# Kernel tuning notes

Hardware: AMD Instinct MI355X
Metric: run time of the kernel (lower is better)

## Reference

```python
import jax, jax.numpy as jnp
import numpy as np

N_NODES = 100000
N_EDGES = 1600000
IN_C, HID_C, OUT_C = 128, 256, 128


def setup_inputs() -> dict:
    key = jax.random.key(0)
    ks = jax.random.split(key, 8)
    x = jax.random.normal(ks[0], (N_NODES, IN_C), dtype=jnp.float32)
    edge_row = jax.random.randint(ks[1], (N_EDGES,), 0, N_NODES, dtype=jnp.int32)
    edge_col = jax.random.randint(ks[2], (N_EDGES,), 0, N_NODES, dtype=jnp.int32)
    # normalized adjacency values (e.g. D^-1/2 A D^-1/2 entries), positive
    edge_vals = jax.random.uniform(ks[3], (N_EDGES,), dtype=jnp.float32) * 0.1
    # torch Linear weights: y = x @ W.T + b (xavier scale)
    W1 = jax.random.normal(ks[4], (HID_C, IN_C), dtype=jnp.float32) * (2.0 / (IN_C + HID_C)) ** 0.5
    b1 = jnp.zeros((HID_C,), dtype=jnp.float32)
    W2 = jax.random.normal(ks[5], (HID_C, HID_C), dtype=jnp.float32) * (1.0 / HID_C) ** 0.5
    b2 = jnp.zeros((HID_C,), dtype=jnp.float32)
    W3 = jax.random.normal(ks[6], (OUT_C, HID_C), dtype=jnp.float32) * (2.0 / (HID_C + OUT_C)) ** 0.5
    b3 = jnp.zeros((OUT_C,), dtype=jnp.float32)
    return {"x": x, "edge_row": edge_row, "edge_col": edge_col, "edge_vals": edge_vals,
            "W1": W1, "b1": b1, "W2": W2, "b2": b2, "W3": W3, "b3": b3}


def reference(x, edge_row, edge_col, edge_vals, W1, b1, W2, b2, W3, b3):
    n = x.shape[0]

    def spmm(h):
        # out[i] = sum over edges e with row[e]==i of vals[e] * h[col[e]]
        msgs = h[edge_col] * edge_vals[:, None]          # [E, C]
        return jax.ops.segment_sum(msgs, edge_row, num_segments=n)

    h = jax.nn.relu(spmm(x) @ W1.T + b1)                 # GCNConv 1 + relu
    h = jax.nn.relu(spmm(h) @ W2.T + b2)                 # GCNConv 2 + relu
    h = spmm(h) @ W3.T + b3                              # GCNConv 3 (no act)
    # F.normalize: L2 along dim=1 with eps clamp 1e-12
    norm = jnp.linalg.norm(h, axis=1, keepdims=True)
    return h / jnp.maximum(norm, 1e-12)
```

## Files before the change

kernel.cpp:

```cpp
#include <hip/hip_runtime.h>
#include <hip/hip_bf16.h>

#define N_NODES 100000
#define N_EDGES 1600000
#define IN_C 128
#define HID_C 256
#define OUT_C 128

typedef __attribute__((ext_vector_type(8))) short bf16x8;
typedef __attribute__((ext_vector_type(4))) float f32x4;
typedef __attribute__((ext_vector_type(2))) float f32x2;

static __device__ __forceinline__ short f2bf(float f) {
    union { float f; unsigned u; } x{f};
    unsigned r = (x.u + 0x7fffu + ((x.u >> 16) & 1u)) >> 16;
    return (short)r;
}
static __device__ __forceinline__ f32x2 bfpair(unsigned d) {
    union { unsigned u; float f; } lo, hi;
    lo.u = d << 16;
    hi.u = d & 0xffff0000u;
    return f32x2{lo.f, hi.f};
}

__global__ void hist_rank(const int* __restrict__ rows, int* __restrict__ deg,
                          int* __restrict__ rank, int E)
{
    int e = blockIdx.x * blockDim.x + threadIdx.x;
    if (e < E) rank[e] = atomicAdd(&deg[rows[e]], 1);
}

#define SCAN_BLOCK 256
#define SCAN_ELEMS 1024

__global__ __launch_bounds__(SCAN_BLOCK) void scan1(const int* __restrict__ deg,
                                                    int* __restrict__ excl,
                                                    int* __restrict__ bsum, int N)
{
    __shared__ int sh[SCAN_BLOCK];
    int t = threadIdx.x;
    int base = blockIdx.x * SCAN_ELEMS + t * 4;
    int v[4];
    #pragma unroll
    for (int i = 0; i < 4; ++i) {
        int idx = base + i;
        v[i] = (idx < N) ? deg[idx] : 0;
    }
    int s = v[0] + v[1] + v[2] + v[3];
    sh[t] = s;
    __syncthreads();
    for (int d = 1; d < SCAN_BLOCK; d <<= 1) {
        int add = (t >= d) ? sh[t - d] : 0;
        __syncthreads();
        sh[t] += add;
        __syncthreads();
    }
    int p = sh[t] - s;
    #pragma unroll
    for (int i = 0; i < 4; ++i) {
        int idx = base + i;
        if (idx < N) excl[idx] = p;
        p += v[i];
    }
    if (t == SCAN_BLOCK - 1) bsum[blockIdx.x] = sh[t];
}

__global__ void scan2(const int* __restrict__ bsum, int* __restrict__ boff, int NB)
{
    __shared__ int sh[128];
    int t = threadIdx.x;
    int v = (t < NB) ? bsum[t] : 0;
    sh[t] = v;
    __syncthreads();
    for (int d = 1; d < 128; d <<= 1) {
        int add = (t >= d) ? sh[t - d] : 0;
        __syncthreads();
        sh[t] += add;
        __syncthreads();
    }
    if (t < NB) boff[t] = sh[t] - v;
}

__global__ void scan3(int* __restrict__ row_start, const int* __restrict__ boff, int N, int E)
{
    int i = blockIdx.x * blockDim.x + threadIdx.x;
    if (i < N) {
        row_start[i] = row_start[i] + boff[i >> 10];
    } else if (i == N) {
        row_start[N] = E;
    }
}

__global__ void scatter_edges(const int* __restrict__ rows, const int* __restrict__ cols,
                              const float* __restrict__ vals, const int* __restrict__ row_start,
                              const int* __restrict__ rank, int2* __restrict__ epk, int E)
{
    int e = blockIdx.x * blockDim.x + threadIdx.x;
    if (e < E) {
        int pos = row_start[rows[e]] + rank[e];
        epk[pos] = int2{cols[e], __float_as_int(vals[e])};
    }
}

__global__ void cast_all(const float* __restrict__ s0, short* __restrict__ d0, int n0,
                         const float* __restrict__ s1, short* __restrict__ d1, int n1,
                         const float* __restrict__ s2, short* __restrict__ d2, int n2,
                         const float* __restrict__ s3, short* __restrict__ d3, int n3)
{
    int i = (blockIdx.x * blockDim.x + threadIdx.x) * 4;
    const float* s; short* d;
    if (i < n0) { s = s0; d = d0; }
    else if ((i -= n0) < n1) { s = s1; d = d1; }
    else if ((i -= n1) < n2) { s = s2; d = d2; }
    else if ((i -= n2) < n3) { s = s3; d = d3; }
    else return;
    float4 v = *(const float4*)(s + i);
    *(short4*)(d + i) = short4{f2bf(v.x), f2bf(v.y), f2bf(v.z), f2bf(v.w)};
}

template<int B, int ND>
static __device__ __forceinline__ void spmm_batch(
    const unsigned* __restrict__ Hb, const int2* __restrict__ epk,
    int j, int loff, f32x2* acc)
{
    int2 e[B];
    #pragma unroll
    for (int b = 0; b < B; ++b) e[b] = epk[j + b];
    uint2 g[B];
    #pragma unroll
    for (int b = 0; b < B; ++b) {
        const unsigned* p = Hb + (size_t)e[b].x * (64 * ND) + loff;
        if constexpr (ND == 2) g[b] = *(const uint2*)p;
        else                   g[b].x = *p;
    }
    #pragma unroll
    for (int b = 0; b < B; ++b) {
        float v = __int_as_float(e[b].y);
        acc[0] += v * bfpair(g[b].x);
        if constexpr (ND == 2) acc[1] += v * bfpair(g[b].y);
    }
}

template<int C, int MODE>
__global__ __launch_bounds__(256) void spmm_gather(
    const short* __restrict__ H, const int* __restrict__ row_start,
    const int2* __restrict__ epk, void* __restrict__ outv,
    const float* __restrict__ bias, int N)
{
    constexpr int PL = C / 64;
    constexpr int ND = PL / 2;
    int wid = threadIdx.x >> 6;
    int lane = threadIdx.x & 63;
    int row = blockIdx.x * 4 + wid;
    if (row >= N) return;
    int j = row_start[row];
    int end = row_start[row + 1];
    const unsigned* Hb = (const unsigned*)H;
    const int loff = lane * ND;

    f32x2 acc[ND];
    #pragma unroll
    for (int d = 0; d < ND; ++d) acc[d] = f32x2{0.f, 0.f};

    for (; j + 8 <= end; j += 8) spmm_batch<8, ND>(Hb, epk, j, loff, acc);
    if (j + 4 <= end) { spmm_batch<4, ND>(Hb, epk, j, loff, acc); j += 4; }
    if (j + 2 <= end) { spmm_batch<2, ND>(Hb, epk, j, loff, acc); j += 2; }
    if (j < end)      { spmm_batch<1, ND>(Hb, epk, j, loff, acc); }

    if constexpr (MODE == 0) {
        unsigned od[ND];
        #pragma unroll
        for (int d = 0; d < ND; ++d)
            od[d] = (unsigned)(unsigned short)f2bf(acc[d].x)
                  | ((unsigned)(unsigned short)f2bf(acc[d].y) << 16);
        unsigned* orow = (unsigned*)outv + (size_t)row * (64 * ND) + loff;
        if constexpr (ND == 2) *(uint2*)orow = uint2{od[0], od[1]};
        else                   *orow = od[0];
    } else {
        int ch = lane * 2;
        float o0 = acc[0].x + bias[ch];
        float o1 = acc[0].y + bias[ch + 1];
        float ss = o0 * o0 + o1 * o1;
        #pragma unroll
        for (int d = 1; d < 64; d <<= 1)
            ss += __shfl_xor(ss, d);
        float s = 1.0f / fmaxf(sqrtf(ss), 1e-12f);
        *(float2*)((float*)outv + (size_t)row * C + ch) = float2{o0 * s, o1 * s};
    }
}

template<int K, int M, bool RELU, bool BIAS>
__global__ __launch_bounds__(256) void gemm_bf16(
    const short* __restrict__ A, const short* __restrict__ W,
    const float* __restrict__ bias, short* __restrict__ Y, int N)
{
    constexpr int BK = 32;
    constexpr int PAD = 8;
    __shared__ short As[128][BK + PAD];
    __shared__ short Ws[64][BK + PAD];

    const int tid = threadIdx.x;
    const int wid = tid >> 6;
    const int lane = tid & 63;
    const int wm = wid & 1;
    const int wn = wid >> 1;
    const int l15 = lane & 15;
    const int quad = lane >> 4;
    const int bn = blockIdx.x * 128;
    const int bm = blockIdx.y * 64;

    f32x4 acc[4][2] = {};

    for (int k0 = 0; k0 < K; k0 += BK) {
        #pragma unroll
        for (int c = 0; c < 2; ++c) {
            int chunk = tid + c * 256;
            int row = chunk >> 2;
            int koff = (chunk & 3) * 8;
            int gr = bn + row;
            ulonglong2 v = {0ull, 0ull};
            if (gr < N) v = *(const ulonglong2*)(A + (size_t)gr * K + k0 + koff);
            *(ulonglong2*)&As[row][koff] = v;
        }
        {
            int row = tid >> 2;
            int koff = (tid & 3) * 8;
            ulonglong2 v = *(const ulonglong2*)(W + (size_t)(bm + row) * K + k0 + koff);
            *(ulonglong2*)&Ws[row][koff] = v;
        }
        __syncthreads();

        bf16x8 aF[4], bF[2];
        #pragma unroll
        for (int mt = 0; mt < 4; ++mt)
            aF[mt] = *(const bf16x8*)&As[wm * 64 + mt * 16 + l15][quad * 8];
        #pragma unroll
        for (int nt = 0; nt < 2; ++nt)
            bF[nt] = *(const bf16x8*)&Ws[wn * 32 + nt * 16 + l15][quad * 8];

        #pragma unroll
        for (int mt = 0; mt < 4; ++mt)
            #pragma unroll
            for (int nt = 0; nt < 2; ++nt)
                acc[mt][nt] = __builtin_amdgcn_mfma_f32_16x16x32_bf16(
                    aF[mt], bF[nt], acc[mt][nt], 0, 0, 0);
        __syncthreads();
    }

    #pragma unroll
    for (int nt = 0; nt < 2; ++nt) {
        int col = bm + wn * 32 + nt * 16 + l15;
        float bv = BIAS ? bias[col] : 0.f;
        #pragma unroll
        for (int mt = 0; mt < 4; ++mt) {
            int row0 = bn + wm * 64 + mt * 16 + quad * 4;
            #pragma unroll
            for (int r = 0; r < 4; ++r) {
                int row = row0 + r;
                if (row < N) {
                    float v = acc[mt][nt][r] + bv;
                    if (RELU) v = fmaxf(v, 0.f);
                    Y[(size_t)row * M + col] = f2bf(v);
                }
            }
        }
    }
}

extern "C" void kernel_launch(void* const* d_in, const int* in_sizes, int n_in,
                              void* d_out, int out_size, void* d_ws, size_t ws_size,
                              hipStream_t stream) {
    const float* x        = (const float*)d_in[0];
    const int*   edge_row = (const int*)d_in[1];
    const int*   edge_col = (const int*)d_in[2];
    const float* edge_val = (const float*)d_in[3];
    const float* W1       = (const float*)d_in[4];
    const float* b1       = (const float*)d_in[5];
    const float* W2       = (const float*)d_in[6];
    const float* b2       = (const float*)d_in[7];
    const float* W3       = (const float*)d_in[8];
    const float* b3       = (const float*)d_in[9];
    float* out = (float*)d_out;

    const int N = N_NODES, E = N_EDGES;
    const int NB = (N + SCAN_ELEMS - 1) / SCAN_ELEMS;

    short* xbf = (short*)d_ws;
    short* Hbf = xbf + (size_t)N * IN_C;
    short* Gbf = Hbf + (size_t)N * HID_C;
    short* W1b = Gbf + (size_t)N * HID_C;
    short* W2b = W1b + HID_C * IN_C;
    short* W3b = W2b + HID_C * HID_C;
    int* deg = (int*)(((uintptr_t)(W3b + OUT_C * HID_C) + 15) & ~(uintptr_t)15);
    int* row_start = deg + N;
    int* rank      = row_start + (N + 1);
    int* bsum      = rank + E;
    int* boff      = bsum + 128;
    int2* epk      = (int2*)(((uintptr_t)(boff + 128) + 15) & ~(uintptr_t)15);

    hipMemsetAsync(deg, 0, N * sizeof(int), stream);
    hist_rank<<<(E + 255) / 256, 256, 0, stream>>>(edge_row, deg, rank, E);
    scan1<<<NB, SCAN_BLOCK, 0, stream>>>(deg, row_start, bsum, N);
    scan2<<<1, 128, 0, stream>>>(bsum, boff, NB);
    scan3<<<(N + 256) / 256, 256, 0, stream>>>(row_start, boff, N, E);
    scatter_edges<<<(E + 255) / 256, 256, 0, stream>>>(edge_row, edge_col, edge_val,
                                                       row_start, rank, epk, E);

    {
        int n0 = N * IN_C, n1 = HID_C * IN_C, n2 = HID_C * HID_C, n3 = OUT_C * HID_C;
        int total4 = (n0 + n1 + n2 + n3) / 4;
        cast_all<<<(total4 + 255) / 256, 256, 0, stream>>>(
            x, xbf, n0, W1, W1b, n1, W2, W2b, n2, W3, W3b, n3);
    }

    const int spmm_grid = (N + 3) / 4;
    const int gemm_gx = (N + 127) / 128;

    spmm_gather<IN_C, 0><<<spmm_grid, 256, 0, stream>>>(
        xbf, row_start, epk, Hbf, nullptr, N);
    gemm_bf16<IN_C, HID_C, true, true><<<dim3(gemm_gx, HID_C / 64), 256, 0, stream>>>(
        Hbf, W1b, b1, Gbf, N);

    spmm_gather<HID_C, 0><<<spmm_grid, 256, 0, stream>>>(
        Gbf, row_start, epk, Hbf, nullptr, N);
    gemm_bf16<HID_C, HID_C, true, true><<<dim3(gemm_gx, HID_C / 64), 256, 0, stream>>>(
        Hbf, W2b, b2, Gbf, N);

    gemm_bf16<HID_C, OUT_C, false, false><<<dim3(gemm_gx, OUT_C / 64), 256, 0, stream>>>(
        Gbf, W3b, nullptr, Hbf, N);
    spmm_gather<OUT_C, 2><<<spmm_grid, 256, 0, stream>>>(
        Hbf, row_start, epk, out, b3, N);
}
```

Baseline: 598.1 us.

## Fuse scan kernels and scatter with cast, remap GEMM block order

The separate block-offset scan kernel is merged into scan3, with each block recomputing the 128-entry prefix in shared memory. The edge scatter and the bf16 cast are merged into one launch. GEMM launches switch to a 1D grid that visits all output-column tiles for groups of 8 row tiles before moving on, so A rows are reused while they are still in cache. This removes two kernel launches, at the cost of redundant per-block prefix work and GEMM blocks that exit early in the padded grid.

```diff
diff --git a/kernel.cpp b/kernel.cpp
--- a/kernel.cpp
+++ b/kernel.cpp
@@ -65,57 +65,52 @@
     if (t == SCAN_BLOCK - 1) bsum[blockIdx.x] = sh[t];
 }
 
-__global__ void scan2(const int* __restrict__ bsum, int* __restrict__ boff, int NB)
-{
-    __shared__ int sh[128];
+__global__ void scan3(int* __restrict__ row_start, const int* __restrict__ bsum,
+                      int NB, int N, int E)
+{
+    __shared__ int pref[128];
     int t = threadIdx.x;
-    int v = (t < NB) ? bsum[t] : 0;
-    sh[t] = v;
+    if (t < 128) pref[t] = (t < NB) ? bsum[t] : 0;
     __syncthreads();
     for (int d = 1; d < 128; d <<= 1) {
-        int add = (t >= d) ? sh[t - d] : 0;
-        __syncthreads();
-        sh[t] += add;
-        __syncthreads();
-    }
-    if (t < NB) boff[t] = sh[t] - v;
-}
-
-__global__ void scan3(int* __restrict__ row_start, const int* __restrict__ boff, int N, int E)
-{
-    int i = blockIdx.x * blockDim.x + threadIdx.x;
+        int add = (t < 128 && t >= d) ? pref[t - d] : 0;
+        __syncthreads();
+        if (t < 128) pref[t] += add;
+        __syncthreads();
+    }
+    int i = blockIdx.x * blockDim.x + t;
     if (i < N) {
-        row_start[i] = row_start[i] + boff[i >> 10];
+        int b = i >> 10;
+        row_start[i] += (b == 0) ? 0 : pref[b - 1];
     } else if (i == N) {
         row_start[N] = E;
     }
 }
 
-__global__ void scatter_edges(const int* __restrict__ rows, const int* __restrict__ cols,
-                              const float* __restrict__ vals, const int* __restrict__ row_start,
-                              const int* __restrict__ rank, int2* __restrict__ epk, int E)
-{
-    int e = blockIdx.x * blockDim.x + threadIdx.x;
-    if (e < E) {
-        int pos = row_start[rows[e]] + rank[e];
-        epk[pos] = int2{cols[e], __float_as_int(vals[e])};
-    }
-}
-
-__global__ void cast_all(const float* __restrict__ s0, short* __restrict__ d0, int n0,
-                         const float* __restrict__ s1, short* __restrict__ d1, int n1,
-                         const float* __restrict__ s2, short* __restrict__ d2, int n2,
-                         const float* __restrict__ s3, short* __restrict__ d3, int n3)
-{
-    int i = (blockIdx.x * blockDim.x + threadIdx.x) * 4;
-    const float* s; short* d;
-    if (i < n0) { s = s0; d = d0; }
-    else if ((i -= n0) < n1) { s = s1; d = d1; }
-    else if ((i -= n1) < n2) { s = s2; d = d2; }
-    else if ((i -= n2) < n3) { s = s3; d = d3; }
-    else return;
-    float4 v = *(const float4*)(s + i);
-    *(short4*)(d + i) = short4{f2bf(v.x), f2bf(v.y), f2bf(v.z), f2bf(v.w)};
+__global__ void scatter_cast(const int* __restrict__ rows, const int* __restrict__ cols,
+                             const float* __restrict__ vals, const int* __restrict__ row_start,
+                             const int* __restrict__ rank, int2* __restrict__ epk, int E,
+                             const float* __restrict__ s0, short* __restrict__ d0, int n0,
+                             const float* __restrict__ s1, short* __restrict__ d1, int n1,
+                             const float* __restrict__ s2, short* __restrict__ d2, int n2,
+                             const float* __restrict__ s3, short* __restrict__ d3, int n3)
+{
+    int idx = blockIdx.x * blockDim.x + threadIdx.x;
+    if (idx < E) {
+        int pos = row_start[rows[idx]] + rank[idx];
+        epk[pos] = int2{cols[idx], __float_as_int(vals[idx])};
+    } else {
+        int i = (idx - E) * 4;
+        int castN = n0 + n1 + n2 + n3;
+        if (i >= castN) return;
+        const float* s; short* d;
+        if (i < n0) { s = s0; d = d0; }
+        else if ((i -= n0) < n1) { s = s1; d = d1; }
+        else if ((i -= n1) < n2) { s = s2; d = d2; }
+        else { i -= n2; s = s3; d = d3; }
+        float4 v = *(const float4*)(s + i);
+        *(short4*)(d + i) = short4{f2bf(v.x), f2bf(v.y), f2bf(v.z), f2bf(v.w)};
+    }
 }
 
 template<int B, int ND>
@@ -194,10 +189,15 @@
     const short* __restrict__ A, const short* __restrict__ W,
     const float* __restrict__ bias, short* __restrict__ Y, int N)
 {
+    constexpr int MBLK = M / 64;
     constexpr int BK = 32;
     constexpr int PAD = 8;
     __shared__ short As[128][BK + PAD];
     __shared__ short Ws[64][BK + PAD];
+
+    const int id = blockIdx.x;
+    const int bx = (id / (8 * MBLK)) * 8 + (id & 7);
+    const int by = (id >> 3) & (MBLK - 1);
 
     const int tid = threadIdx.x;
     const int wid = tid >> 6;
@@ -206,8 +206,8 @@
     const int wn = wid >> 1;
     const int l15 = lane & 15;
     const int quad = lane >> 4;
-    const int bn = blockIdx.x * 128;
-    const int bm = blockIdx.y * 64;
+    const int bn = bx * 128;
+    const int bm = by * 64;
 
     f32x4 acc[4][2] = {};
 
@@ -295,38 +295,34 @@
     int* row_start = deg + N;
     int* rank      = row_start + (N + 1);
     int* bsum      = rank + E;
-    int* boff      = bsum + 128;
-    int2* epk      = (int2*)(((uintptr_t)(boff + 128) + 15) & ~(uintptr_t)15);
+    int2* epk      = (int2*)(((uintptr_t)(bsum + 128) + 15) & ~(uintptr_t)15);
 
     hipMemsetAsync(deg, 0, N * sizeof(int), stream);
     hist_rank<<<(E + 255) / 256, 256, 0, stream>>>(edge_row, deg, rank, E);
     scan1<<<NB, SCAN_BLOCK, 0, stream>>>(deg, row_start, bsum, N);
-    scan2<<<1, 128, 0, stream>>>(bsum, boff, NB);
-    scan3<<<(N + 256) / 256, 256, 0, stream>>>(row_start, boff, N, E);
-    scatter_edges<<<(E + 255) / 256, 256, 0, stream>>>(edge_row, edge_col, edge_val,
-                                                       row_start, rank, epk, E);
-
+    scan3<<<(N + 256) / 256, 256, 0, stream>>>(row_start, bsum, NB, N, E);
     {
         int n0 = N * IN_C, n1 = HID_C * IN_C, n2 = HID_C * HID_C, n3 = OUT_C * HID_C;
-        int total4 = (n0 + n1 + n2 + n3) / 4;
-        cast_all<<<(total4 + 255) / 256, 256, 0, stream>>>(
+        int total = E + (n0 + n1 + n2 + n3) / 4;
+        scatter_cast<<<(total + 255) / 256, 256, 0, stream>>>(
+            edge_row, edge_col, edge_val, row_start, rank, epk, E,
             x, xbf, n0, W1, W1b, n1, W2, W2b, n2, W3, W3b, n3);
     }
 
     const int spmm_grid = (N + 3) / 4;
-    const int gemm_gx = (N + 127) / 128;
+    const int GXP = ((N + 127) / 128 + 7) & ~7;
 
     spmm_gather<IN_C, 0><<<spmm_grid, 256, 0, stream>>>(
         xbf, row_start, epk, Hbf, nullptr, N);
-    gemm_bf16<IN_C, HID_C, true, true><<<dim3(gemm_gx, HID_C / 64), 256, 0, stream>>>(
+    gemm_bf16<IN_C, HID_C, true, true><<<GXP * (HID_C / 64), 256, 0, stream>>>(
         Hbf, W1b, b1, Gbf, N);
 
     spmm_gather<HID_C, 0><<<spmm_grid, 256, 0, stream>>>(
         Gbf, row_start, epk, Hbf, nullptr, N);
-    gemm_bf16<HID_C, HID_C, true, true><<<dim3(gemm_gx, HID_C / 64), 256, 0, stream>>>(
+    gemm_bf16<HID_C, HID_C, true, true><<<GXP * (HID_C / 64), 256, 0, stream>>>(
         Hbf, W2b, b2, Gbf, N);
 
-    gemm_bf16<HID_C, OUT_C, false, false><<<dim3(gemm_gx, OUT_C / 64), 256, 0, stream>>>(
+    gemm_bf16<HID_C, OUT_C, false, false><<<GXP * (OUT_C / 64), 256, 0, stream>>>(
         Gbf, W3b, nullptr, Hbf, N);
     spmm_gather<OUT_C, 2><<<spmm_grid, 256, 0, stream>>>(
         Hbf, row_start, epk, out, b3, N);
```

Result: faster. 566.9 us (-5.2%).
